# Performance work log

Hardware: AMD Instinct MI355X
Metric: run time of the kernel (lower is better)

Reference implementation:

```python
import jax, jax.numpy as jnp
import numpy as np
import math

H = 768
NH = 12
D = H // NH


def setup_inputs() -> dict:
    key = jax.random.key(0)
    ks = jax.random.split(key, 13)
    B, S = 1, 384
    s = 0.02
    inp = {
        "hidden_states": jax.random.normal(ks[0], (B, S, H), jnp.float32),
        "attention_mask": jnp.zeros((B, 1, 1, S), jnp.float32),
        "pos_emb": jax.random.normal(ks[1], (B, S, S, H), jnp.float32),
        "Wq": jax.random.normal(ks[2], (H, H), jnp.float32) * s,
        "bq": jnp.zeros((H,), jnp.float32),
        "Wk": jax.random.normal(ks[3], (H, H), jnp.float32) * s,
        "bk": jnp.zeros((H,), jnp.float32),
        "Wv": jax.random.normal(ks[4], (H, H), jnp.float32) * s,
        "bv": jnp.zeros((H,), jnp.float32),
        "Wpk": jax.random.normal(ks[5], (H, H), jnp.float32) * s,
        "bpk": jnp.zeros((H,), jnp.float32),
        "Wpq": jax.random.normal(ks[6], (H, H), jnp.float32) * s,
        "bpq": jnp.zeros((H,), jnp.float32),
    }
    return inp


def reference(hidden_states, attention_mask, pos_emb,
              Wq, bq, Wk, bk, Wv, bv, Wpk, bpk, Wpq, bpq):
    B, S, Hd = hidden_states.shape
    split = lambda x: x.reshape(B, S, NH, D).transpose(0, 2, 1, 3)  # -> (B, h, S, d)
    q = split(hidden_states @ Wq + bq)
    k = split(hidden_states @ Wk + bk)
    v = split(hidden_states @ Wv + bv)

    # content-to-content
    c2c = jnp.einsum('bhid,bhjd->bhij', q, k)

    # per-pair position projections: (B,S,S,H) -> (B,S,S,h,d)
    pos_key = (pos_emb @ Wpk + bpk).reshape(B, S, S, NH, D)
    pos_query = (pos_emb @ Wpq + bpq).reshape(B, S, S, NH, D)

    # content-to-position: q[b,h,i,:] . pos_key[b,i,j,h,:]
    c2p = jnp.einsum('bhid,bijhd->bhij', q, pos_key)
    # position-to-content: pos_query[b,j,i,h,:] . k[b,h,j,:]
    p2c = jnp.einsum('bjihd,bhjd->bhij', pos_query, k)

    scores = (c2c + c2p + p2c) / math.sqrt(D) + attention_mask
    probs = jax.nn.softmax(scores, axis=-1)  # dropout is identity (p=0 / eval)
    ctx = jnp.einsum('bhij,bhjd->bhid', probs, v)
    return ctx.transpose(0, 2, 1, 3).reshape(B, S, Hd)
```

## Files before the change

### kernel.cpp

```cpp
#include <hip/hip_runtime.h>
#include <math.h>

#define SEQ 384
#define HDIM 768
#define NHEAD 12
#define DHEAD 64
#define GI 4

__global__ __launch_bounds__(256)
void qkv_gemm(const float* __restrict__ X,
              const float* __restrict__ Wq, const float* __restrict__ bq,
              const float* __restrict__ Wk, const float* __restrict__ bk,
              const float* __restrict__ Wv, const float* __restrict__ bv,
              float* __restrict__ q, float* __restrict__ k, float* __restrict__ v)
{
    __shared__ float Xs[128 * 68];
    const int z = blockIdx.z;
    const float* W    = (z == 0) ? Wq : (z == 1) ? Wk : Wv;
    const float* bias = (z == 0) ? bq : (z == 1) ? bk : bv;
    float* out        = (z == 0) ? q  : (z == 1) ? k  : v;

    const int m0 = blockIdx.x * 64;
    const int n0 = blockIdx.y * 64;
    const int tid = threadIdx.x;
    const int ty = tid / 16, tx = tid % 16;

    const int lm = tid >> 2;
    const int lc = (tid & 3) * 4;

    float acc[4][4] = {};

    for (int k0 = 0; k0 < HDIM; k0 += 128) {
        float4 xa[8];
        #pragma unroll
        for (int it = 0; it < 8; it++)
            xa[it] = *(const float4*)&X[(size_t)(m0 + lm) * HDIM + k0 + it * 16 + lc];
        __syncthreads();
        #pragma unroll
        for (int it = 0; it < 8; it++) {
            const int kk = it * 16 + lc;
            Xs[(kk + 0) * 68 + lm] = xa[it].x;
            Xs[(kk + 1) * 68 + lm] = xa[it].y;
            Xs[(kk + 2) * 68 + lm] = xa[it].z;
            Xs[(kk + 3) * 68 + lm] = xa[it].w;
        }
        __syncthreads();
        const float* Wp = &W[(size_t)k0 * HDIM + n0 + 4 * tx];
        #pragma unroll 8
        for (int kk = 0; kk < 128; kk++) {
            float4 b4 = *(const float4*)&Wp[(size_t)kk * HDIM];
            float4 a4 = *(const float4*)&Xs[kk * 68 + 4 * ty];
            float a[4] = {a4.x, a4.y, a4.z, a4.w};
            float b[4] = {b4.x, b4.y, b4.z, b4.w};
            #pragma unroll
            for (int ia = 0; ia < 4; ia++)
                #pragma unroll
                for (int ib = 0; ib < 4; ib++)
                    acc[ia][ib] = fmaf(a[ia], b[ib], acc[ia][ib]);
        }
    }
    float4 bv4 = *(const float4*)&bias[n0 + 4 * tx];
    #pragma unroll
    for (int ia = 0; ia < 4; ia++) {
        float4 o;
        o.x = acc[ia][0] + bv4.x; o.y = acc[ia][1] + bv4.y;
        o.z = acc[ia][2] + bv4.z; o.w = acc[ia][3] + bv4.w;
        *(float4*)&out[(size_t)(m0 + 4 * ty + ia) * HDIM + n0 + 4 * tx] = o;
    }
}

__global__ __launch_bounds__(256)
void proj_all(const float* __restrict__ q, const float* __restrict__ k,
              const float* __restrict__ Wpk, const float* __restrict__ Wpq,
              const float* __restrict__ bpq, const float* __restrict__ bpk,
              const float* __restrict__ mask,
              float* __restrict__ qp, float* __restrict__ kp,
              float* __restrict__ CC)
{
    __shared__ float As[64][68];
    __shared__ float Bs[64][68];
    __shared__ float cterm_s;
    const int z = blockIdx.z;
    const int tid = threadIdx.x;
    const int dg = tid % 16, row = tid / 16;
    const int ty = tid / 16, tx = tid % 16;

    if (z < 24) {
        const int h = z % NHEAD;
        const int s = z / NHEAD;
        const float* Asrc = s ? k   : q;
        const float* Wsrc = s ? Wpq : Wpk;
        float* out        = s ? kp  : qp;
        const int i0 = blockIdx.x * 64, e0 = blockIdx.y * 64;

        #pragma unroll
        for (int r = 0; r < 4; r++) {
            const int rr = r * 16 + row;
            float4 a4 = *(const float4*)&Asrc[(size_t)(i0 + rr) * HDIM + h * 64 + dg * 4];
            float4 b4 = *(const float4*)&Wsrc[(size_t)(e0 + rr) * HDIM + h * 64 + dg * 4];
            As[dg * 4 + 0][rr] = a4.x; As[dg * 4 + 1][rr] = a4.y;
            As[dg * 4 + 2][rr] = a4.z; As[dg * 4 + 3][rr] = a4.w;
            Bs[dg * 4 + 0][rr] = b4.x; Bs[dg * 4 + 1][rr] = b4.y;
            Bs[dg * 4 + 2][rr] = b4.z; Bs[dg * 4 + 3][rr] = b4.w;
        }
        __syncthreads();

        float acc[4][4] = {};
        #pragma unroll 4
        for (int d = 0; d < 64; d++) {
            float4 a4 = *(const float4*)&As[d][4 * ty];
            float4 b4 = *(const float4*)&Bs[d][4 * tx];
            float a[4] = {a4.x, a4.y, a4.z, a4.w};
            float b[4] = {b4.x, b4.y, b4.z, b4.w};
            #pragma unroll
            for (int ia = 0; ia < 4; ia++)
                #pragma unroll
                for (int ib = 0; ib < 4; ib++)
                    acc[ia][ib] = fmaf(a[ia], b[ib], acc[ia][ib]);
        }
        const int e = e0 + 4 * tx;
        const int off = (e >> 5) * 384 + ((e >> 4) & 1) * 192 + h * 16 + (e & 15);
        #pragma unroll
        for (int ia = 0; ia < 4; ia++) {
            float4 o = make_float4(acc[ia][0], acc[ia][1], acc[ia][2], acc[ia][3]);
            *(float4*)&out[(size_t)(i0 + 4 * ty + ia) * (NHEAD * HDIM) + off] = o;
        }
    } else {
        if (blockIdx.y >= 6) return;
        const int h  = z - 24;
        const int i0 = blockIdx.x * 64, j0 = blockIdx.y * 64;

        const float4 bq4 = *(const float4*)&bpq[h * 64 + dg * 4];
        const float4 bk4 = *(const float4*)&bpk[h * 64 + dg * 4];
        #pragma unroll
        for (int r = 0; r < 4; r++) {
            const int rr = r * 16 + row;
            float4 q4 = *(const float4*)&q[(size_t)(i0 + rr) * HDIM + h * 64 + dg * 4];
            float4 k4 = *(const float4*)&k[(size_t)(j0 + rr) * HDIM + h * 64 + dg * 4];
            As[dg * 4 + 0][rr] = q4.x + bq4.x; As[dg * 4 + 1][rr] = q4.y + bq4.y;
            As[dg * 4 + 2][rr] = q4.z + bq4.z; As[dg * 4 + 3][rr] = q4.w + bq4.w;
            Bs[dg * 4 + 0][rr] = k4.x + bk4.x; Bs[dg * 4 + 1][rr] = k4.y + bk4.y;
            Bs[dg * 4 + 2][rr] = k4.z + bk4.z; Bs[dg * 4 + 3][rr] = k4.w + bk4.w;
        }
        if (tid < 64) {
            float pc = bpq[h * 64 + tid] * bpk[h * 64 + tid];
            #pragma unroll
            for (int o = 32; o; o >>= 1) pc += __shfl_xor(pc, o);
            if (tid == 0) cterm_s = pc;
        }
        __syncthreads();

        float acc[4][4] = {};
        #pragma unroll 4
        for (int d = 0; d < 64; d++) {
            float4 a4 = *(const float4*)&As[d][4 * ty];
            float4 b4 = *(const float4*)&Bs[d][4 * tx];
            float a[4] = {a4.x, a4.y, a4.z, a4.w};
            float b[4] = {b4.x, b4.y, b4.z, b4.w};
            #pragma unroll
            for (int ia = 0; ia < 4; ia++)
                #pragma unroll
                for (int ib = 0; ib < 4; ib++)
                    acc[ia][ib] = fmaf(a[ia], b[ib], acc[ia][ib]);
        }
        const float cterm = cterm_s;
        const float4 m4 = *(const float4*)&mask[j0 + 4 * tx];
        #pragma unroll
        for (int ia = 0; ia < 4; ia++) {
            float4 o;
            o.x = (acc[ia][0] - cterm) * 0.125f + m4.x;
            o.y = (acc[ia][1] - cterm) * 0.125f + m4.y;
            o.z = (acc[ia][2] - cterm) * 0.125f + m4.z;
            o.w = (acc[ia][3] - cterm) * 0.125f + m4.w;
            *(float4*)&CC[((size_t)h * SEQ + i0 + 4 * ty + ia) * SEQ + j0 + 4 * tx] = o;
        }
    }
}

__global__ __launch_bounds__(256, 3)
void scores_pos(const float* __restrict__ pe, const float* __restrict__ qp,
                const float* __restrict__ kp,
                float* __restrict__ A1, float* __restrict__ P2T)
{
    __shared__ float lds[32 * 200];
    const int i    = blockIdx.x;
    const int jh   = blockIdx.y;
    const int tid  = threadIdx.x;
    const int lane = tid & 63;
    const int wave = tid >> 6;
    const int rgu = __builtin_amdgcn_readfirstlane(wave >> 1);
    const int esu = __builtin_amdgcn_readfirstlane(wave & 1);

    const float* pebase = pe + ((size_t)i * SEQ + jh * 192) * HDIM;
    const float* wb = (rgu ? kp : qp) + (size_t)i * NHEAD * HDIM;

    const int wr  = tid >> 3;
    const int wec = tid & 7;

    float acc[12][3] = {};
    float4 ga[6], gb[6];

    auto loadc = [&](float4* g, int c) {
        const int e0 = c * 32;
        #pragma unroll
        for (int rnd = 0; rnd < 3; rnd++) {
            const int jb = rnd * 64 + wr * 2;
            g[2 * rnd + 0] = *(const float4*)&pebase[(size_t)jb * HDIM + e0 + wec * 4];
            g[2 * rnd + 1] = *(const float4*)&pebase[(size_t)(jb + 1) * HDIM + e0 + wec * 4];
        }
    };
    auto writec = [&](const float4* g) {
        #pragma unroll
        for (int rnd = 0; rnd < 3; rnd++) {
            const int jb = rnd * 64 + wr * 2;
            const float4 g0 = g[2 * rnd], g1 = g[2 * rnd + 1];
            *(float2*)&lds[(wec * 4 + 0) * 200 + jb] = make_float2(g0.x, g1.x);
            *(float2*)&lds[(wec * 4 + 1) * 200 + jb] = make_float2(g0.y, g1.y);
            *(float2*)&lds[(wec * 4 + 2) * 200 + jb] = make_float2(g0.z, g1.z);
            *(float2*)&lds[(wec * 4 + 3) * 200 + jb] = make_float2(g0.w, g1.w);
        }
    };
    auto compute = [&](int c) {
        const float* wc = wb + c * 384 + esu * 192;
        #pragma unroll 4
        for (int ee = 0; ee < 16; ee++) {
            const int ei = esu * 16 + ee;
            float2 p2 = *(const float2*)&lds[ei * 200 + 2 * lane];
            float  p1 = lds[ei * 200 + 128 + lane];
            #pragma unroll
            for (int r = 0; r < 12; r++) {
                const float w = wc[r * 16 + ee];
                acc[r][0] = fmaf(w, p2.x, acc[r][0]);
                acc[r][1] = fmaf(w, p2.y, acc[r][1]);
                acc[r][2] = fmaf(w, p1,   acc[r][2]);
            }
        }
    };

    loadc(ga, 0);
    #pragma unroll 1
    for (int cc = 0; cc < 12; cc++) {
        loadc(gb, 2 * cc + 1);
        __syncthreads();
        writec(ga);
        __syncthreads();
        if (cc < 11) loadc(ga, 2 * cc + 2);
        compute(2 * cc);
        __syncthreads();
        writec(gb);
        __syncthreads();
        compute(2 * cc + 1);
    }

    __syncthreads();
    if (esu == 1) {
        #pragma unroll
        for (int r = 0; r < 12; r++) {
            const int row = rgu * 12 + r;
            *(float2*)&lds[row * 200 + 2 * lane] = make_float2(acc[r][0], acc[r][1]);
            lds[row * 200 + 128 + lane] = acc[r][2];
        }
    }
    __syncthreads();
    if (esu == 0) {
        #pragma unroll
        for (int r = 0; r < 12; r++) {
            const int row = rgu * 12 + r;
            float2 o2 = *(const float2*)&lds[row * 200 + 2 * lane];
            float  o1 = lds[row * 200 + 128 + lane];
            o2.x += acc[r][0]; o2.y += acc[r][1]; o1 += acc[r][2];
            *(float2*)&lds[row * 200 + 2 * lane] = o2;
            lds[row * 200 + 128 + lane] = o1;
        }
    }
    __syncthreads();

    for (int t = tid; t < 24 * 48; t += 256) {
        const int row = t / 48;
        const int c4  = (t % 48) * 4;
        float4 o = *(const float4*)&lds[row * 200 + c4];
        o.x *= 0.125f; o.y *= 0.125f; o.z *= 0.125f; o.w *= 0.125f;
        float* dst = (row < 12)
            ? &A1[((size_t)row * SEQ + i) * SEQ + jh * 192 + c4]
            : &P2T[((size_t)(row - 12) * SEQ + i) * SEQ + jh * 192 + c4];
        *(float4*)dst = o;
    }
}

__global__ __launch_bounds__(384)
void attn_out(const float* __restrict__ CC, const float* __restrict__ A1,
              const float* __restrict__ P2T, const float* __restrict__ v,
              float* __restrict__ out)
{
    const int i0 = blockIdx.x * GI, h = blockIdx.y;
    const int tid = threadIdx.x;
    __shared__ float p_s[GI][SEQ];
    __shared__ float redm[GI][6], reds[GI][6];
    __shared__ float redvf[GI][24 * 64];

    const int lane = tid & 63, w = tid >> 6;

    float4 t4 = *(const float4*)&P2T[((size_t)h * SEQ + tid) * SEQ + i0];
    float tt[GI] = {t4.x, t4.y, t4.z, t4.w};
    float sc[GI];
    #pragma unroll
    for (int g = 0; g < GI; g++) {
        const size_t off = ((size_t)h * SEQ + i0 + g) * SEQ + tid;
        sc[g] = CC[off] + A1[off] + tt[g];
    }

    #pragma unroll
    for (int g = 0; g < GI; g++) {
        float m = sc[g];
        #pragma unroll
        for (int o = 32; o; o >>= 1) m = fmaxf(m, __shfl_xor(m, o));
        if (lane == 0) redm[g][w] = m;
    }
    __syncthreads();
    float SUMv[GI];
    #pragma unroll
    for (int g = 0; g < GI; g++) {
        float m = redm[g][0];
        #pragma unroll
        for (int t = 1; t < 6; t++) m = fmaxf(m, redm[g][t]);
        float p = __expf(sc[g] - m);
        float sum = p;
        #pragma unroll
        for (int o = 32; o; o >>= 1) sum += __shfl_xor(sum, o);
        if (lane == 0) reds[g][w] = sum;
        p_s[g][tid] = p;
    }
    __syncthreads();
    #pragma unroll
    for (int g = 0; g < GI; g++)
        SUMv[g] = reds[g][0] + reds[g][1] + reds[g][2] +
                  reds[g][3] + reds[g][4] + reds[g][5];

    const int dq = lane & 15, jsub = lane >> 4;
    const int j0 = w * 64;
    float4 av[GI] = {};
    #pragma unroll 4
    for (int jj = 0; jj < 16; jj++) {
        const int j = j0 + jj * 4 + jsub;
        float4 v4 = *(const float4*)&v[(size_t)j * HDIM + h * 64 + dq * 4];
        #pragma unroll
        for (int g = 0; g < GI; g++) {
            const float pj = p_s[g][j];
            av[g].x = fmaf(pj, v4.x, av[g].x); av[g].y = fmaf(pj, v4.y, av[g].y);
            av[g].z = fmaf(pj, v4.z, av[g].z); av[g].w = fmaf(pj, v4.w, av[g].w);
        }
    }
    #pragma unroll
    for (int g = 0; g < GI; g++)
        *(float4*)&redvf[g][(w * 4 + jsub) * 64 + dq * 4] = av[g];
    __syncthreads();
    if (tid < 64) {
        #pragma unroll
        for (int g = 0; g < GI; g++) {
            float o = 0.f;
            #pragma unroll
            for (int r = 0; r < 24; r++) o += redvf[g][r * 64 + tid];
            out[(size_t)(i0 + g) * HDIM + h * 64 + tid] = o / SUMv[g];
        }
    }
}

extern "C" void kernel_launch(void* const* d_in, const int* in_sizes, int n_in,
                              void* d_out, int out_size, void* d_ws, size_t ws_size,
                              hipStream_t stream)
{
    const float* hs   = (const float*)d_in[0];
    const float* mask = (const float*)d_in[1];
    const float* pe   = (const float*)d_in[2];
    const float* Wq   = (const float*)d_in[3];
    const float* bq   = (const float*)d_in[4];
    const float* Wk   = (const float*)d_in[5];
    const float* bk   = (const float*)d_in[6];
    const float* Wv   = (const float*)d_in[7];
    const float* bv   = (const float*)d_in[8];
    const float* Wpk  = (const float*)d_in[9];
    const float* bpk  = (const float*)d_in[10];
    const float* Wpq  = (const float*)d_in[11];
    const float* bpq  = (const float*)d_in[12];

    float* ws = (float*)d_ws;
    const size_t SZ_QKV = (size_t)SEQ * HDIM;
    const size_t SZ_QP  = (size_t)SEQ * NHEAD * HDIM;
    const size_t SZ_SC  = (size_t)NHEAD * SEQ * SEQ;
    float* q   = ws;
    float* k   = q  + SZ_QKV;
    float* v   = k  + SZ_QKV;
    float* qp  = v  + SZ_QKV;
    float* kp  = qp + SZ_QP;
    float* A1  = kp + SZ_QP;
    float* P2T = A1 + SZ_SC;
    float* CC  = P2T + SZ_SC;

    qkv_gemm<<<dim3(6, 12, 3), 256, 0, stream>>>(hs, Wq, bq, Wk, bk, Wv, bv, q, k, v);
    proj_all<<<dim3(6, 12, 36), 256, 0, stream>>>(q, k, Wpk, Wpq, bpq, bpk, mask,
                                                  qp, kp, CC);
    scores_pos<<<dim3(SEQ, 2), 256, 0, stream>>>(pe, qp, kp, A1, P2T);
    attn_out<<<dim3(SEQ / GI, NHEAD), 384, 0, stream>>>(CC, A1, P2T, v, (float*)d_out);
}
```

Baseline: 783.7 us.

## Double-buffer LDS in scores_pos and prefetch X tiles in qkv_gemm

The scores_pos kernel moves from a single LDS tile to two LDS buffers. Chunk writes now overlap compute on the other buffer, which cuts the barriers per iteration from four to two. The qkv_gemm kernel prefetches the next X tile into registers while it computes the current one. The cost is double the LDS in scores_pos (about 51KB per block), which may reduce occupancy below the launch-bounds target of 3 blocks. The pipeline is also more complex, with a risk of read-after-write hazards.

```diff
diff --git a/kernel.cpp b/kernel.cpp
--- a/kernel.cpp
+++ b/kernel.cpp
@@ -6,6 +6,7 @@
 #define NHEAD 12
 #define DHEAD 64
 #define GI 4
+#define LDSB 6400
 
 __global__ __launch_bounds__(256)
 void qkv_gemm(const float* __restrict__ X,
@@ -29,12 +30,13 @@
     const int lc = (tid & 3) * 4;
 
     float acc[4][4] = {};
+    float4 xa[8];
+
+    #pragma unroll
+    for (int it = 0; it < 8; it++)
+        xa[it] = *(const float4*)&X[(size_t)(m0 + lm) * HDIM + it * 16 + lc];
 
     for (int k0 = 0; k0 < HDIM; k0 += 128) {
-        float4 xa[8];
-        #pragma unroll
-        for (int it = 0; it < 8; it++)
-            xa[it] = *(const float4*)&X[(size_t)(m0 + lm) * HDIM + k0 + it * 16 + lc];
         __syncthreads();
         #pragma unroll
         for (int it = 0; it < 8; it++) {
@@ -45,6 +47,11 @@
             Xs[(kk + 3) * 68 + lm] = xa[it].w;
         }
         __syncthreads();
+        if (k0 + 128 < HDIM) {
+            #pragma unroll
+            for (int it = 0; it < 8; it++)
+                xa[it] = *(const float4*)&X[(size_t)(m0 + lm) * HDIM + k0 + 128 + it * 16 + lc];
+        }
         const float* Wp = &W[(size_t)k0 * HDIM + n0 + 4 * tx];
         #pragma unroll 8
         for (int kk = 0; kk < 128; kk++) {
@@ -182,7 +189,7 @@
                 const float* __restrict__ kp,
                 float* __restrict__ A1, float* __restrict__ P2T)
 {
-    __shared__ float lds[32 * 200];
+    __shared__ float lds[2 * LDSB];
     const int i    = blockIdx.x;
     const int jh   = blockIdx.y;
     const int tid  = threadIdx.x;
@@ -209,24 +216,24 @@
             g[2 * rnd + 1] = *(const float4*)&pebase[(size_t)(jb + 1) * HDIM + e0 + wec * 4];
         }
     };
-    auto writec = [&](const float4* g) {
+    auto writec = [&](float* buf, const float4* g) {
         #pragma unroll
         for (int rnd = 0; rnd < 3; rnd++) {
             const int jb = rnd * 64 + wr * 2;
             const float4 g0 = g[2 * rnd], g1 = g[2 * rnd + 1];
-            *(float2*)&lds[(wec * 4 + 0) * 200 + jb] = make_float2(g0.x, g1.x);
-            *(float2*)&lds[(wec * 4 + 1) * 200 + jb] = make_float2(g0.y, g1.y);
-            *(float2*)&lds[(wec * 4 + 2) * 200 + jb] = make_float2(g0.z, g1.z);
-            *(float2*)&lds[(wec * 4 + 3) * 200 + jb] = make_float2(g0.w, g1.w);
+            *(float2*)&buf[(wec * 4 + 0) * 200 + jb] = make_float2(g0.x, g1.x);
+            *(float2*)&buf[(wec * 4 + 1) * 200 + jb] = make_float2(g0.y, g1.y);
+            *(float2*)&buf[(wec * 4 + 2) * 200 + jb] = make_float2(g0.z, g1.z);
+            *(float2*)&buf[(wec * 4 + 3) * 200 + jb] = make_float2(g0.w, g1.w);
         }
     };
-    auto compute = [&](int c) {
+    auto compute = [&](const float* buf, int c) {
         const float* wc = wb + c * 384 + esu * 192;
         #pragma unroll 4
         for (int ee = 0; ee < 16; ee++) {
             const int ei = esu * 16 + ee;
-            float2 p2 = *(const float2*)&lds[ei * 200 + 2 * lane];
-            float  p1 = lds[ei * 200 + 128 + lane];
+            float2 p2 = *(const float2*)&buf[ei * 200 + 2 * lane];
+            float  p1 = buf[ei * 200 + 128 + lane];
             #pragma unroll
             for (int r = 0; r < 12; r++) {
                 const float w = wc[r * 16 + ee];
@@ -237,28 +244,34 @@
         }
     };
 
+    float* buf0 = lds;
+    float* buf1 = lds + LDSB;
+
     loadc(ga, 0);
+    loadc(gb, 1);
+    writec(buf0, ga);
+    __syncthreads();
     #pragma unroll 1
     for (int cc = 0; cc < 12; cc++) {
-        loadc(gb, 2 * cc + 1);
-        __syncthreads();
-        writec(ga);
-        __syncthreads();
-        if (cc < 11) loadc(ga, 2 * cc + 2);
-        compute(2 * cc);
-        __syncthreads();
-        writec(gb);
-        __syncthreads();
-        compute(2 * cc + 1);
-    }
-
-    __syncthreads();
+        const int c0 = 2 * cc, c1 = 2 * cc + 1;
+        if (cc < 11) loadc(ga, c0 + 2);
+        writec(buf1, gb);
+        compute(buf0, c0);
+        __syncthreads();
+        if (cc < 11) {
+            loadc(gb, c1 + 2);
+            writec(buf0, ga);
+        }
+        compute(buf1, c1);
+        __syncthreads();
+    }
+
     if (esu == 1) {
         #pragma unroll
         for (int r = 0; r < 12; r++) {
             const int row = rgu * 12 + r;
-            *(float2*)&lds[row * 200 + 2 * lane] = make_float2(acc[r][0], acc[r][1]);
-            lds[row * 200 + 128 + lane] = acc[r][2];
+            *(float2*)&buf0[row * 200 + 2 * lane] = make_float2(acc[r][0], acc[r][1]);
+            buf0[row * 200 + 128 + lane] = acc[r][2];
         }
     }
     __syncthreads();
@@ -266,11 +279,11 @@
         #pragma unroll
         for (int r = 0; r < 12; r++) {
             const int row = rgu * 12 + r;
-            float2 o2 = *(const float2*)&lds[row * 200 + 2 * lane];
-            float  o1 = lds[row * 200 + 128 + lane];
+            float2 o2 = *(const float2*)&buf0[row * 200 + 2 * lane];
+            float  o1 = buf0[row * 200 + 128 + lane];
             o2.x += acc[r][0]; o2.y += acc[r][1]; o1 += acc[r][2];
-            *(float2*)&lds[row * 200 + 2 * lane] = o2;
-            lds[row * 200 + 128 + lane] = o1;
+            *(float2*)&buf0[row * 200 + 2 * lane] = o2;
+            buf0[row * 200 + 128 + lane] = o1;
         }
     }
     __syncthreads();
@@ -278,7 +291,7 @@
     for (int t = tid; t < 24 * 48; t += 256) {
         const int row = t / 48;
         const int c4  = (t % 48) * 4;
-        float4 o = *(const float4*)&lds[row * 200 + c4];
+        float4 o = *(const float4*)&buf0[row * 200 + c4];
         o.x *= 0.125f; o.y *= 0.125f; o.z *= 0.125f; o.w *= 0.125f;
         float* dst = (row < 12)
             ? &A1[((size_t)row * SEQ + i) * SEQ + jh * 192 + c4]
```

New measurement: 989.3 us. 26.2% more time.
